# Kernel optimization log

Measured on AMD Instinct MI355X. Metric: run time of the kernel, lower is better.

The kernel has to match this reference:

```python
import jax, jax.numpy as jnp
import numpy as np
from jax.scipy.special import logsumexp

TEMPERATURE = 0.1
EPS = 1e-8  # matches torch F.cosine_similarity eps


def setup_inputs() -> dict:
    key = jax.random.key(0)
    k1, k2 = jax.random.split(key)
    N, D, NUM_CLASSES = 8192, 256, 64
    embeddings = jax.random.normal(k1, (N, D), dtype=jnp.float32)
    target = jax.random.randint(k2, (N,), 0, NUM_CLASSES, dtype=jnp.int64)
    return {"embeddings": embeddings, "target": target}


def reference(embeddings, target):
    N = target.shape[0]
    # cosine similarity: normalize rows, then a single GEMM for all pairs
    norms = jnp.linalg.norm(embeddings, axis=-1, keepdims=True)
    e = embeddings / jnp.maximum(norms, EPS)
    sim = (e @ e.T) / TEMPERATURE  # [N, N]

    pos = target[:, None] == target[None, :]  # [N, N] bool, incl. diagonal
    diag = jnp.eye(N, dtype=bool)
    neg_inf = jnp.asarray(-jnp.inf, dtype=sim.dtype)

    # denominator: negatives only (positives masked to -inf)
    lse_neg = logsumexp(jnp.where(pos, neg_inf, sim), axis=1)
    # numerator: positives excluding self (diagonal masked to -inf)
    lse_pos = logsumexp(jnp.where(pos & ~diag, sim, neg_inf), axis=1)

    loss = lse_neg - lse_pos
    return loss.sum()
```

## Files before the change

### kernel.cpp

```cpp
#include <hip/hip_runtime.h>
#include <hip/hip_bf16.h>
#include <stdint.h>
#include <math.h>

#define NROWS 8192
#define DIM   256
#define BJ    256
#define BI    128
#define KCB   128
#define NKC   2
#define NJT   (NROWS/BJ)
#define NIT   (NROWS/BI)
#define NPART (NJT*2)

typedef __attribute__((ext_vector_type(4)))  int   int4v;
typedef __attribute__((ext_vector_type(8)))  int   int8v;
typedef __attribute__((ext_vector_type(16))) float floatx16;

typedef const __attribute__((address_space(1))) uint32_t gas_u32;
typedef __attribute__((address_space(3))) uint32_t las_u32;

#define SCALE_1_16 0x7B7B7B7B
#define L2E10      14.4269504088896f

__device__ __forceinline__ void gload_lds16(const void* g, void* l) {
    __builtin_amdgcn_global_load_lds((gas_u32*)(uintptr_t)g,
                                     (las_u32*)(uintptr_t)l, 16, 0, 0);
}

__global__ __launch_bounds__(256) void normalize_kernel(const float* __restrict__ emb,
                                                        uint32_t* __restrict__ e8,
                                                        float* __restrict__ out)
{
    if (blockIdx.x == 0 && threadIdx.x == 0) *out = 0.f;
    int row  = blockIdx.x * 4 + (threadIdx.x >> 6);
    int lane = threadIdx.x & 63;
    const float4* rowp = (const float4*)(emb + (size_t)row * DIM);
    float4 v = rowp[lane];
    float ss = v.x*v.x + v.y*v.y + v.z*v.z + v.w*v.w;
    #pragma unroll
    for (int off = 32; off > 0; off >>= 1)
        ss += __shfl_xor(ss, off, 64);
    float inv = 16.0f / fmaxf(sqrtf(ss), 1e-8f);
    int r = __builtin_amdgcn_cvt_pk_fp8_f32(v.x * inv, v.y * inv, 0, false);
    r     = __builtin_amdgcn_cvt_pk_fp8_f32(v.z * inv, v.w * inv, r, true);
    e8[(size_t)row * (DIM / 4) + lane] = (uint32_t)r;
}

template<bool DIAG>
__device__ __forceinline__ void epilogue_accum(const floatx16 acc[4][2],
                                               const int* __restrict__ tgt,
                                               int jb0, const int tiv[2], const int ic[2],
                                               float ps[2], float ts[2])
{
    #pragma unroll
    for (int jt = 0; jt < 4; ++jt) {
        #pragma unroll
        for (int rq = 0; rq < 4; ++rq) {
            const int jg = jb0 + jt * 32 + rq * 8;
            const int4v t4 = *(const int4v*)(tgt + jg);
            #pragma unroll
            for (int it = 0; it < 2; ++it) {
                const int tivc = tiv[it];
                #pragma unroll
                for (int r2 = 0; r2 < 4; ++r2) {
                    float v = exp2f(fmaf(L2E10, acc[jt][it][rq * 4 + r2], -L2E10));
                    if (DIAG) {
                        if (jg + r2 == ic[it]) v = 0.f;
                    }
                    ts[it] += v;
                    ps[it] += (t4[r2] == tivc) ? v : 0.f;
                }
            }
        }
    }
}

__global__ __launch_bounds__(256, 2) void tile_kernel(const uint8_t* __restrict__ e8,
                                                      const int* __restrict__ tgt,
                                                      float* __restrict__ pps,
                                                      float* __restrict__ pts)
{
    __shared__ uint8_t sA[BJ * KCB];
    __shared__ uint8_t sB[BI * KCB];

    const int bi   = blockIdx.x;
    const int bj   = blockIdx.y;
    const int tid  = threadIdx.x;
    const int wave = tid >> 6;
    const int lane = tid & 63;
    const int col  = lane & 31;
    const int h    = lane >> 5;

    const int wr = (wave >> 1) * 128;
    const int wc = (wave & 1) * 64;

    floatx16 acc[4][2];
    #pragma unroll
    for (int a = 0; a < 4; ++a)
        #pragma unroll
        for (int b = 0; b < 2; ++b)
            acc[a][b] = (floatx16){0.f,0.f,0.f,0.f,0.f,0.f,0.f,0.f,
                                   0.f,0.f,0.f,0.f,0.f,0.f,0.f,0.f};

    int goffA[8];
    #pragma unroll
    for (int t = 0; t < 8; ++t) {
        int s   = wave * 512 + t * 64 + lane;
        int row = s >> 3;
        int lc  = (s & 7) ^ (row & 7);
        goffA[t] = row * 256 + lc * 16;
    }
    int goffB[4];
    #pragma unroll
    for (int t = 0; t < 4; ++t) {
        int s   = wave * 256 + t * 64 + lane;
        int row = s >> 3;
        int lc  = (s & 7) ^ (row & 7);
        goffB[t] = row * 256 + lc * 16;
    }

    const char* gA = (const char*)(e8 + (size_t)bj * BJ * 256);
    const char* gB = (const char*)(e8 + (size_t)bi * BI * 256);

    const int xr = lane & 7;
    int coff[2][2];
    #pragma unroll
    for (int s = 0; s < 2; ++s)
        #pragma unroll
        for (int c = 0; c < 2; ++c)
            coff[s][c] = ((s * 4 + h * 2 + c) ^ xr) << 4;

    #pragma unroll
    for (int kc = 0; kc < NKC; ++kc) {
        #pragma unroll
        for (int t = 0; t < 8; ++t)
            gload_lds16(gA + goffA[t] + kc * KCB, sA + wave * 8192 + t * 1024);
        #pragma unroll
        for (int t = 0; t < 4; ++t)
            gload_lds16(gB + goffB[t] + kc * KCB, sB + wave * 4096 + t * 1024);
        __syncthreads();

        int8v bfr[2][2];
        #pragma unroll
        for (int it = 0; it < 2; ++it) {
            const uint8_t* pb = sB + (wc + it * 32 + col) * KCB;
            #pragma unroll
            for (int s = 0; s < 2; ++s) {
                int4v lo = *(const int4v*)(pb + coff[s][0]);
                int4v hi = *(const int4v*)(pb + coff[s][1]);
                bfr[s][it] = __builtin_shufflevector(lo, hi, 0, 1, 2, 3, 4, 5, 6, 7);
            }
        }
        #pragma unroll
        for (int jt = 0; jt < 4; ++jt) {
            const uint8_t* pa = sA + (wr + jt * 32 + col) * KCB;
            #pragma unroll
            for (int s = 0; s < 2; ++s) {
                int4v lo = *(const int4v*)(pa + coff[s][0]);
                int4v hi = *(const int4v*)(pa + coff[s][1]);
                int8v af = __builtin_shufflevector(lo, hi, 0, 1, 2, 3, 4, 5, 6, 7);
                #pragma unroll
                for (int it = 0; it < 2; ++it)
                    acc[jt][it] = __builtin_amdgcn_mfma_scale_f32_32x32x64_f8f6f4(
                        af, bfr[s][it], acc[jt][it], 0, 0,
                        0, SCALE_1_16, 0, SCALE_1_16);
            }
        }
        __syncthreads();
    }

    int tiv[2], ic[2];
    #pragma unroll
    for (int it = 0; it < 2; ++it) {
        ic[it]  = bi * BI + wc + it * 32 + col;
        tiv[it] = tgt[ic[it]];
    }

    float ps[2] = {0.f, 0.f};
    float ts[2] = {0.f, 0.f};

    const int jb0 = bj * BJ + wr + h * 4;
    if ((bi >> 1) == bj)
        epilogue_accum<true >(acc, tgt, jb0, tiv, ic, ps, ts);
    else
        epilogue_accum<false>(acc, tgt, jb0, tiv, ic, ps, ts);

    #pragma unroll
    for (int it = 0; it < 2; ++it) {
        ps[it] += __shfl_xor(ps[it], 32, 64);
        ts[it] += __shfl_xor(ts[it], 32, 64);
    }
    if (h == 0) {
        const size_t base = (size_t)(bj * 2 + (wave >> 1)) * NROWS;
        #pragma unroll
        for (int it = 0; it < 2; ++it) {
            pps[base + ic[it]] = ps[it];
            pts[base + ic[it]] = ts[it];
        }
    }
}

__global__ __launch_bounds__(256) void finalize_kernel(const float* __restrict__ pps,
                                                       const float* __restrict__ pts,
                                                       float* __restrict__ out)
{
    const int i = blockIdx.x * 256 + threadIdx.x;
    float sp = 0.f, st = 0.f;
    #pragma unroll 8
    for (int t = 0; t < NPART; ++t) {
        sp += pps[(size_t)t * NROWS + i];
        st += pts[(size_t)t * NROWS + i];
    }
    float ns = st - sp;
    float loss = logf(ns) - logf(sp);
    #pragma unroll
    for (int off = 32; off > 0; off >>= 1)
        loss += __shfl_xor(loss, off, 64);
    __shared__ float w4[4];
    if ((threadIdx.x & 63) == 0) w4[threadIdx.x >> 6] = loss;
    __syncthreads();
    if (threadIdx.x == 0)
        atomicAdd(out, w4[0] + w4[1] + w4[2] + w4[3]);
}

extern "C" void kernel_launch(void* const* d_in, const int* in_sizes, int n_in,
                              void* d_out, int out_size, void* d_ws, size_t ws_size,
                              hipStream_t stream)
{
    (void)in_sizes; (void)n_in; (void)out_size; (void)ws_size;
    const float* emb = (const float*)d_in[0];
    const int*   tgt = (const int*)d_in[1];
    float*       out = (float*)d_out;

    uint32_t* e8  = (uint32_t*)d_ws;
    float*    pps = (float*)((char*)d_ws + (size_t)NROWS * 256);
    float*    pts = pps + (size_t)NPART * NROWS;

    normalize_kernel<<<NROWS / 4, 256, 0, stream>>>(emb, e8, out);

    dim3 grid(NIT, NJT);
    tile_kernel<<<grid, 256, 0, stream>>>((const uint8_t*)e8, tgt, pps, pts);

    finalize_kernel<<<NROWS / 256, 256, 0, stream>>>(pps, pts, out);
}
```

Before: 103.2 us.

## Keep B fragments in registers and double-buffer A tiles across j sub-blocks

Each block now loads its full-K B tile (128 rows × 256 fp8) once and holds the fragments in registers. It then loops over four 128-row A sub-tiles of a 512-row j group. The next A sub-tile is loaded into the other of two LDS buffers while the current one is multiplied, so global-to-LDS traffic overlaps with MFMA and epilogue work. The grid halves in the j dimension and partial-sum slots drop from 64 to 16, which cuts partial-store and finalize reads. The cost is more LDS per block (64 KB), fewer blocks to hide latency, and a smaller per-wave accumulator tile (2x2).

```diff
diff --git a/kernel.cpp b/kernel.cpp
--- a/kernel.cpp
+++ b/kernel.cpp
@@ -5,13 +5,12 @@
 
 #define NROWS 8192
 #define DIM   256
-#define BJ    256
+#define RB    256
 #define BI    128
-#define KCB   128
-#define NKC   2
-#define NJT   (NROWS/BJ)
+#define JBLK  512
+#define NBJS  4
+#define NG    (NROWS/JBLK)
 #define NIT   (NROWS/BI)
-#define NPART (NJT*2)
 
 typedef __attribute__((ext_vector_type(4)))  int   int4v;
 typedef __attribute__((ext_vector_type(8)))  int   int8v;
@@ -48,17 +47,17 @@
 }
 
 template<bool DIAG>
-__device__ __forceinline__ void epilogue_accum(const floatx16 acc[4][2],
-                                               const int* __restrict__ tgt,
-                                               int jb0, const int tiv[2], const int ic[2],
-                                               float ps[2], float ts[2])
-{
-    #pragma unroll
-    for (int jt = 0; jt < 4; ++jt) {
+__device__ __forceinline__ void epi(const floatx16 acc[2][2],
+                                    const int* __restrict__ tgt,
+                                    int jb, const int tiv[2], const int ic[2],
+                                    float ps[2], float ts[2])
+{
+    #pragma unroll
+    for (int jt = 0; jt < 2; ++jt) {
         #pragma unroll
         for (int rq = 0; rq < 4; ++rq) {
-            const int jg = jb0 + jt * 32 + rq * 8;
-            const int4v t4 = *(const int4v*)(tgt + jg);
+            const int jg_ = jb + jt * 32 + rq * 8;
+            const int4v t4 = *(const int4v*)(tgt + jg_);
             #pragma unroll
             for (int it = 0; it < 2; ++it) {
                 const int tivc = tiv[it];
@@ -66,7 +65,7 @@
                 for (int r2 = 0; r2 < 4; ++r2) {
                     float v = exp2f(fmaf(L2E10, acc[jt][it][rq * 4 + r2], -L2E10));
                     if (DIAG) {
-                        if (jg + r2 == ic[it]) v = 0.f;
+                        if (jg_ + r2 == ic[it]) v = 0.f;
                     }
                     ts[it] += v;
                     ps[it] += (t4[r2] == tivc) ? v : 0.f;
@@ -81,110 +80,117 @@
                                                       float* __restrict__ pps,
                                                       float* __restrict__ pts)
 {
-    __shared__ uint8_t sA[BJ * KCB];
-    __shared__ uint8_t sB[BI * KCB];
+    __shared__ uint8_t buf[2][BI * RB];
 
     const int bi   = blockIdx.x;
-    const int bj   = blockIdx.y;
+    const int jg   = blockIdx.y;
     const int tid  = threadIdx.x;
     const int wave = tid >> 6;
     const int lane = tid & 63;
     const int col  = lane & 31;
     const int h    = lane >> 5;
 
-    const int wr = (wave >> 1) * 128;
+    const int wr = (wave >> 1) * 64;
     const int wc = (wave & 1) * 64;
 
-    floatx16 acc[4][2];
-    #pragma unroll
-    for (int a = 0; a < 4; ++a)
-        #pragma unroll
-        for (int b = 0; b < 2; ++b)
-            acc[a][b] = (floatx16){0.f,0.f,0.f,0.f,0.f,0.f,0.f,0.f,
-                                   0.f,0.f,0.f,0.f,0.f,0.f,0.f,0.f};
-
-    int goffA[8];
+    int goff[8];
     #pragma unroll
     for (int t = 0; t < 8; ++t) {
         int s   = wave * 512 + t * 64 + lane;
-        int row = s >> 3;
-        int lc  = (s & 7) ^ (row & 7);
-        goffA[t] = row * 256 + lc * 16;
-    }
-    int goffB[4];
-    #pragma unroll
-    for (int t = 0; t < 4; ++t) {
-        int s   = wave * 256 + t * 64 + lane;
-        int row = s >> 3;
-        int lc  = (s & 7) ^ (row & 7);
-        goffB[t] = row * 256 + lc * 16;
-    }
-
-    const char* gA = (const char*)(e8 + (size_t)bj * BJ * 256);
-    const char* gB = (const char*)(e8 + (size_t)bi * BI * 256);
-
-    const int xr = lane & 7;
-    int coff[2][2];
-    #pragma unroll
-    for (int s = 0; s < 2; ++s)
+        int row = s >> 4;
+        int lc  = (s & 15) ^ (row & 15);
+        goff[t] = row * RB + lc * 16;
+    }
+
+    const char* gB = (const char*)(e8 + (size_t)bi * BI * RB);
+    const char* gA = (const char*)(e8 + (size_t)jg * JBLK * RB);
+
+    #pragma unroll
+    for (int t = 0; t < 8; ++t)
+        gload_lds16(gA + goff[t], buf[0] + wave * 8192 + t * 1024);
+    #pragma unroll
+    for (int t = 0; t < 8; ++t)
+        gload_lds16(gB + goff[t], buf[1] + wave * 8192 + t * 1024);
+    __syncthreads();
+
+    const int xm = col & 15;
+    int poff[4][2];
+    #pragma unroll
+    for (int s = 0; s < 4; ++s)
         #pragma unroll
         for (int c = 0; c < 2; ++c)
-            coff[s][c] = ((s * 4 + h * 2 + c) ^ xr) << 4;
-
-    #pragma unroll
-    for (int kc = 0; kc < NKC; ++kc) {
-        #pragma unroll
-        for (int t = 0; t < 8; ++t)
-            gload_lds16(gA + goffA[t] + kc * KCB, sA + wave * 8192 + t * 1024);
-        #pragma unroll
-        for (int t = 0; t < 4; ++t)
-            gload_lds16(gB + goffB[t] + kc * KCB, sB + wave * 4096 + t * 1024);
-        __syncthreads();
-
-        int8v bfr[2][2];
-        #pragma unroll
-        for (int it = 0; it < 2; ++it) {
-            const uint8_t* pb = sB + (wc + it * 32 + col) * KCB;
-            #pragma unroll
-            for (int s = 0; s < 2; ++s) {
-                int4v lo = *(const int4v*)(pb + coff[s][0]);
-                int4v hi = *(const int4v*)(pb + coff[s][1]);
-                bfr[s][it] = __builtin_shufflevector(lo, hi, 0, 1, 2, 3, 4, 5, 6, 7);
+            poff[s][c] = ((s * 4 + h * 2 + c) ^ xm) << 4;
+
+    int8v bfr[2][4];
+    #pragma unroll
+    for (int it = 0; it < 2; ++it) {
+        const uint8_t* pb = buf[1] + (wc + it * 32 + col) * RB;
+        #pragma unroll
+        for (int s = 0; s < 4; ++s) {
+            int4v lo = *(const int4v*)(pb + poff[s][0]);
+            int4v hi = *(const int4v*)(pb + poff[s][1]);
+            bfr[it][s] = __builtin_shufflevector(lo, hi, 0, 1, 2, 3, 4, 5, 6, 7);
+        }
+    }
+    __syncthreads();
+
+    int tiv[2], ic[2];
+    #pragma unroll
+    for (int it = 0; it < 2; ++it) {
+        ic[it]  = bi * BI + wc + it * 32 + col;
+        tiv[it] = tgt[ic[it]];
+    }
+
+    float ps[2] = {0.f, 0.f};
+    float ts[2] = {0.f, 0.f};
+
+    const int dbi = bi - jg * 4;
+
+    for (int bjs = 0; bjs < NBJS; ++bjs) {
+        if (bjs < NBJS - 1) {
+            const char* gAn = gA + (size_t)(bjs + 1) * BI * RB;
+            #pragma unroll
+            for (int t = 0; t < 8; ++t)
+                gload_lds16(gAn + goff[t], buf[(bjs + 1) & 1] + wave * 8192 + t * 1024);
+        }
+
+        const uint8_t* ab = buf[bjs & 1];
+        floatx16 acc[2][2];
+        #pragma unroll
+        for (int a = 0; a < 2; ++a)
+            #pragma unroll
+            for (int b = 0; b < 2; ++b)
+                acc[a][b] = (floatx16){0.f,0.f,0.f,0.f,0.f,0.f,0.f,0.f,
+                                       0.f,0.f,0.f,0.f,0.f,0.f,0.f,0.f};
+
+        #pragma unroll
+        for (int s = 0; s < 4; ++s) {
+            int8v af[2];
+            #pragma unroll
+            for (int jt = 0; jt < 2; ++jt) {
+                const uint8_t* pa = ab + (wr + jt * 32 + col) * RB;
+                int4v lo = *(const int4v*)(pa + poff[s][0]);
+                int4v hi = *(const int4v*)(pa + poff[s][1]);
+                af[jt] = __builtin_shufflevector(lo, hi, 0, 1, 2, 3, 4, 5, 6, 7);
             }
-        }
-        #pragma unroll
-        for (int jt = 0; jt < 4; ++jt) {
-            const uint8_t* pa = sA + (wr + jt * 32 + col) * KCB;
-            #pragma unroll
-            for (int s = 0; s < 2; ++s) {
-                int4v lo = *(const int4v*)(pa + coff[s][0]);
-                int4v hi = *(const int4v*)(pa + coff[s][1]);
-                int8v af = __builtin_shufflevector(lo, hi, 0, 1, 2, 3, 4, 5, 6, 7);
+            #pragma unroll
+            for (int jt = 0; jt < 2; ++jt)
                 #pragma unroll
                 for (int it = 0; it < 2; ++it)
                     acc[jt][it] = __builtin_amdgcn_mfma_scale_f32_32x32x64_f8f6f4(
-                        af, bfr[s][it], acc[jt][it], 0, 0,
+                        af[jt], bfr[it][s], acc[jt][it], 0, 0,
                         0, SCALE_1_16, 0, SCALE_1_16);
-            }
-        }
-        __syncthreads();
-    }
-
-    int tiv[2], ic[2];
-    #pragma unroll
-    for (int it = 0; it < 2; ++it) {
-        ic[it]  = bi * BI + wc + it * 32 + col;
-        tiv[it] = tgt[ic[it]];
-    }
-
-    float ps[2] = {0.f, 0.f};
-    float ts[2] = {0.f, 0.f};
-
-    const int jb0 = bj * BJ + wr + h * 4;
-    if ((bi >> 1) == bj)
-        epilogue_accum<true >(acc, tgt, jb0, tiv, ic, ps, ts);
-    else
-        epilogue_accum<false>(acc, tgt, jb0, tiv, ic, ps, ts);
+        }
+
+        const int jb = jg * JBLK + bjs * BI + wr + h * 4;
+        if (bjs == dbi)
+            epi<true >(acc, tgt, jb, tiv, ic, ps, ts);
+        else
+            epi<false>(acc, tgt, jb, tiv, ic, ps, ts);
+
+        if (bjs < NBJS - 1)
+            __syncthreads();
+    }
 
     #pragma unroll
     for (int it = 0; it < 2; ++it) {
@@ -192,7 +198,7 @@
         ts[it] += __shfl_xor(ts[it], 32, 64);
     }
     if (h == 0) {
-        const size_t base = (size_t)(bj * 2 + (wave >> 1)) * NROWS;
+        const size_t base = (size_t)jg * NROWS;
         #pragma unroll
         for (int it = 0; it < 2; ++it) {
             pps[base + ic[it]] = ps[it];
@@ -207,8 +213,8 @@
 {
     const int i = blockIdx.x * 256 + threadIdx.x;
     float sp = 0.f, st = 0.f;
-    #pragma unroll 8
-    for (int t = 0; t < NPART; ++t) {
+    #pragma unroll
+    for (int t = 0; t < NG; ++t) {
         sp += pps[(size_t)t * NROWS + i];
         st += pts[(size_t)t * NROWS + i];
     }
@@ -234,12 +240,12 @@
     float*       out = (float*)d_out;
 
     uint32_t* e8  = (uint32_t*)d_ws;
-    float*    pps = (float*)((char*)d_ws + (size_t)NROWS * 256);
-    float*    pts = pps + (size_t)NPART * NROWS;
+    float*    pps = (float*)((char*)d_ws + (size_t)NROWS * RB);
+    float*    pts = pps + (size_t)NG * NROWS;
 
     normalize_kernel<<<NROWS / 4, 256, 0, stream>>>(emb, e8, out);
 
-    dim3 grid(NIT, NJT);
+    dim3 grid(NIT, NG);
     tile_kernel<<<grid, 256, 0, stream>>>((const uint8_t*)e8, tgt, pps, pts);
 
     finalize_kernel<<<NROWS / 256, 256, 0, stream>>>(pps, pts, out);
```

After: 98.00 us. -5.0%, faster.
